# Kernel optimization log

Hardware: AMD Instinct MI355X
Metric: run time of the kernel (lower is better)

The kernel has to match this reference:

```python
import jax, jax.numpy as jnp
import numpy as np

N = 100000   # nodes
E = 220000   # directed edges (each branch)
H = 128      # hidden_dim
OUT = 1      # output_dim
G = 4096     # num graphs in batch
PE = 5       # laplacian eigenvector PE dims
VOCAB = 28   # atom types


def gcn_conv(x, src, dst, W, b, n):
    # PyG GCNConv: x' = D^-1/2 (A + I) D^-1/2 (X W) + b
    h = x @ W
    deg = jax.ops.segment_sum(jnp.ones(src.shape[0], x.dtype), dst, num_segments=n) + 1.0
    dinv = jax.lax.rsqrt(deg)
    coef = dinv[src] * dinv[dst]                                    # [E]
    agg = jax.ops.segment_sum(h[src] * coef[:, None], dst, num_segments=n)
    agg = agg + h * (dinv * dinv)[:, None]                          # self-loop term
    return agg + b


def gcn2(x, edge_index, W1, b1, W2, b2, n):
    # PyG GCN model, num_layers=2: conv -> relu -> conv
    src, dst = edge_index[0], edge_index[1]
    h = jax.nn.relu(gcn_conv(x, src, dst, W1, b1, n))
    return gcn_conv(h, src, dst, W2, b2, n)


def setup_inputs() -> dict:
    key = jax.random.key(0)
    ks = jax.random.split(key, 16)
    s = 0.1
    return {
        "node_tokens": jax.random.randint(ks[0], (N, 1), 0, VOCAB),
        "pe": jax.random.normal(ks[1], (N, PE), jnp.float32),
        "edge_index": jax.random.randint(ks[2], (2, E), 0, N),
        "vr_edge_index": jax.random.randint(ks[3], (2, E), 0, N),
        "batch": jnp.sort(jax.random.randint(ks[4], (N,), 0, G)),
        "embed_table": jax.random.normal(ks[5], (VOCAB, H), jnp.float32) * s,
        "Wt": jax.random.normal(ks[6], (PE, H), jnp.float32) * s,
        "bt": jnp.zeros((H,), jnp.float32),
        "W1": jax.random.normal(ks[7], (H, H), jnp.float32) * s,
        "b1": jnp.zeros((H,), jnp.float32),
        "W2": jax.random.normal(ks[8], (H, OUT), jnp.float32) * s,
        "b2": jnp.zeros((OUT,), jnp.float32),
        "Wv1": jax.random.normal(ks[9], (H, H), jnp.float32) * s,
        "bv1": jnp.zeros((H,), jnp.float32),
        "Wv2": jax.random.normal(ks[10], (H, OUT), jnp.float32) * s,
        "bv2": jnp.zeros((OUT,), jnp.float32),
    }


def reference(node_tokens, pe, edge_index, vr_edge_index, batch, embed_table,
              Wt, bt, W1, b1, W2, b2, Wv1, bv1, Wv2, bv2):
    # embed_x(data.x.long()).squeeze(1) + lin_trans(pe)
    x = embed_table[node_tokens[:, 0]] + (pe @ Wt + bt)             # [N, H]
    x1 = gcn2(x, edge_index, W1, b1, W2, b2, N)                     # [N, OUT]
    xv = gcn2(x, vr_edge_index, Wv1, bv1, Wv2, bv2, N)              # [N, OUT]
    x1 = x1 + xv
    y_hat = jax.ops.segment_sum(x1, batch, num_segments=G)          # [G, OUT]
    y_hat = jnp.squeeze(y_hat, axis=-1)                             # [G]
    return (y_hat, x)
```

## Files before the change

### kernel.cpp

```cpp
#include <hip/hip_runtime.h>

#define NN 100000
#define NE 220000
#define HD 128
#define NG 4096
#define NPE 5
#define NB_SCAN ((NN + 255) / 256)
#define NBX4 ((NN * HD / 4) / 256)
#define NT16 (NN / 16)
#define NBGEMM 1024
#define NBW 128
#define NBZ ((2 * NN + 255) / 256)
#define NBE2 14
#define NBD ((2 * NE + 255) / 256)

typedef unsigned int uint;
typedef unsigned short ushort;
typedef __attribute__((ext_vector_type(8))) short bf16x8;
typedef __attribute__((ext_vector_type(4))) float f32x4;

__device__ __forceinline__ float bf2f(uint u16) {
    return __uint_as_float(u16 << 16);
}
__device__ __forceinline__ ushort f2bf(float f) {
    uint u = __float_as_uint(f);
    u += 0x7fffu + ((u >> 16) & 1u);
    return (ushort)(u >> 16);
}

__global__ void k_prep0(const float* __restrict__ W1, const float* __restrict__ Wv1,
                        const float* __restrict__ embed, const float* __restrict__ bt,
                        ushort* __restrict__ Wcat, int* __restrict__ cnt,
                        float* __restrict__ embed2) {
    int b = blockIdx.x;
    if (b < NBW) {
        int t = b * 256 + threadIdx.x;
        int f = t >> 7, k = t & 127;
        const float* W = (f < HD) ? W1 : Wv1;
        Wcat[t] = f2bf(W[k * HD + (f & 127)]);
    } else if (b < NBW + NBZ) {
        int t = (b - NBW) * 256 + threadIdx.x;
        if (t < 2 * NN) cnt[t] = 0;
    } else {
        int t = (b - NBW - NBZ) * 256 + threadIdx.x;
        if (t < 28 * 128) embed2[t] = embed[t] + bt[t & 127];
    }
}

__global__ void k_front(const int* __restrict__ tok, const float* __restrict__ pe,
                        const float* __restrict__ embed2, const float* __restrict__ Wtr,
                        float* __restrict__ x, ushort* __restrict__ xb,
                        const int* __restrict__ ei, const int* __restrict__ vei,
                        int* __restrict__ cnt, int* __restrict__ rank) {
    int b = blockIdx.x;
    if (b < NBX4) {
        int idx = b * 256 + threadIdx.x;
        int n = idx >> 5, q = idx & 31;
        int t = tok[n];
        float4 acc = ((const float4*)(embed2 + (size_t)t * HD))[q];
        const float* pen = pe + n * NPE;
#pragma unroll
        for (int k = 0; k < NPE; ++k) {
            float p = pen[k];
            float4 wv = ((const float4*)(Wtr + k * HD))[q];
            acc.x += p * wv.x; acc.y += p * wv.y;
            acc.z += p * wv.z; acc.w += p * wv.w;
        }
        ((float4*)x)[idx] = acc;
        uint2 pk;
        pk.x = (uint)f2bf(acc.x) | ((uint)f2bf(acc.y) << 16);
        pk.y = (uint)f2bf(acc.z) | ((uint)f2bf(acc.w) << 16);
        ((uint2*)xb)[idx] = pk;
    } else {
        int t = (b - NBX4) * 256 + threadIdx.x;
        if (t < 2 * NE) {
            int br = t >= NE;
            int e = t - br * NE;
            const int* S = br ? vei : ei;
            rank[t] = atomicAdd(&cnt[br * NN + S[NE + e]], 1);
        }
    }
}

__global__ __launch_bounds__(256) void k_gemm_scan1(
        const ushort* __restrict__ xb, const ushort* __restrict__ Wt,
        ushort* __restrict__ H,
        const int* __restrict__ cnt, int* __restrict__ off,
        int* __restrict__ bsum, float* __restrict__ dinv, float* __restrict__ y) {
    __shared__ int s[256];
    int b = blockIdx.x;
    if (b < 2 * NB_SCAN) {
        int tid = threadIdx.x;
        int gid = b * 256 + tid;
        if (gid < NG) y[gid] = 0.f;
        int br = b / NB_SCAN;
        int blk = b % NB_SCAN;
        int i = blk * 256 + tid;
        int v = (i < NN) ? cnt[br * NN + i] : 0;
        if (i < NN) dinv[br * NN + i] = rsqrtf((float)v + 1.0f);
        s[tid] = v;
        __syncthreads();
        for (int d = 1; d < 256; d <<= 1) {
            int t = (tid >= d) ? s[tid - d] : 0;
            __syncthreads();
            s[tid] += t;
            __syncthreads();
        }
        if (i < NN) off[br * NN + i] = s[tid] - v;
        if (tid == 255) bsum[br * 512 + blk] = s[255];
    } else {
        int w = threadIdx.x >> 6;
        int lane = threadIdx.x & 63;
        int m = lane & 15, quad = lane >> 4;
        const ushort* Wbase = Wt + ((size_t)(w * 4) * 16 + m) * 128 + quad * 8;
        bf16x8 wf[4][4];
#pragma unroll
        for (int j = 0; j < 4; ++j)
#pragma unroll
            for (int kc = 0; kc < 4; ++kc)
                wf[j][kc] = *(const bf16x8*)(Wbase + (size_t)j * 16 * 128 + kc * 32);

        for (int t = b - 2 * NB_SCAN; t < NT16; t += NBGEMM) {
            int n = t * 16 + m;
            const ushort* Arow = xb + (size_t)n * HD + quad * 8;
            bf16x8 xf[4];
#pragma unroll
            for (int kc = 0; kc < 4; ++kc)
                xf[kc] = *(const bf16x8*)(Arow + kc * 32);
            f32x4 acc[4] = {};
#pragma unroll
            for (int j = 0; j < 4; ++j)
#pragma unroll
                for (int kc = 0; kc < 4; ++kc)
                    acc[j] = __builtin_amdgcn_mfma_f32_16x16x32_bf16(wf[j][kc], xf[kc],
                                                                     acc[j], 0, 0, 0);
#pragma unroll
            for (int j = 0; j < 4; ++j) {
                f32x4 a = acc[j];
                uint2 pk;
                pk.x = (uint)f2bf(a[0]) | ((uint)f2bf(a[1]) << 16);
                pk.y = (uint)f2bf(a[2]) | ((uint)f2bf(a[3]) << 16);
                *(uint2*)&H[(size_t)n * 256 + (w * 4 + j) * 16 + quad * 4] = pk;
            }
        }
    }
}

__global__ void k_scan3(const int* __restrict__ off, const int* __restrict__ bsum,
                        const int* __restrict__ cnt, int2* __restrict__ off2) {
    __shared__ int s[256];
    int br = blockIdx.x / NB_SCAN;
    int blk = blockIdx.x % NB_SCAN;
    int tid = threadIdx.x;
    int v = 0;
    if (tid < blk) v = bsum[br * 512 + tid];
    if (tid + 256 < blk) v += bsum[br * 512 + tid + 256];
    s[tid] = v;
#pragma unroll
    for (int d = 128; d > 0; d >>= 1) {
        __syncthreads();
        if (tid < d) s[tid] += s[tid + d];
    }
    __syncthreads();
    int pre = s[0];
    int i = blk * 256 + tid;
    if (i < NN) {
        int o = off[br * NN + i] + pre;
        int2 pr;
        pr.x = o;
        pr.y = o + cnt[br * NN + i];
        off2[br * NN + i] = pr;
    }
}

__global__ void k_scatter(const int* __restrict__ ei, const int* __restrict__ vei,
                          const int* __restrict__ rank, const float* __restrict__ dinv,
                          const int2* __restrict__ off2, int2* __restrict__ ent) {
    int t = blockIdx.x * blockDim.x + threadIdx.x;
    if (t >= 2 * NE) return;
    int br = t >= NE;
    int e = t - br * NE;
    const int* S = br ? vei : ei;
    int s = S[e], d = S[NE + e];
    int pos = off2[br * NN + d].x + rank[t];
    int2 rec;
    rec.x = s;
    rec.y = __float_as_int(dinv[br * NN + s] * dinv[br * NN + d]);
    ent[br * NE + pos] = rec;
}

__global__ void k_gather_ep(const ushort* __restrict__ H, const float* __restrict__ dinv,
                            const int2* __restrict__ off2,
                            const int2* __restrict__ ent,
                            const float* __restrict__ b1, const float* __restrict__ bv1,
                            const float* __restrict__ W2, const float* __restrict__ Wv2,
                            float* __restrict__ z) {
    int wid = threadIdx.x >> 6;
    int lane = threadIdx.x & 63;
    int half = lane >> 5;
    int l = lane & 31;
    int task = blockIdx.x * 8 + wid * 2 + half;
    int br = task >= NN;
    int n = task - br * NN;

    const int2* en = ent + br * NE;
    size_t hoff = (size_t)br * 128;

    int2 pr = off2[br * NN + n];
    int p0 = pr.x, p1 = pr.y;

    float dv = dinv[br * NN + n];
    uint2 u = *(const uint2*)(H + (size_t)n * 256 + hoff + l * 4);
    float c = dv * dv;
    float a0 = bf2f(u.x & 0xffffu) * c, a1 = bf2f(u.x >> 16) * c;
    float a2 = bf2f(u.y & 0xffffu) * c, a3 = bf2f(u.y >> 16) * c;

    for (int p = p0; p < p1; p += 4) {
        int2 e0 = en[p], e1 = en[p + 1], e2 = en[p + 2], e3 = en[p + 3];
        int s0 = e0.x;
        int s1 = (p + 1 < p1) ? e1.x : n;
        int s2 = (p + 2 < p1) ? e2.x : n;
        int s3 = (p + 3 < p1) ? e3.x : n;
        float c0 = __int_as_float(e0.y);
        float c1 = (p + 1 < p1) ? __int_as_float(e1.y) : 0.f;
        float c2 = (p + 2 < p1) ? __int_as_float(e2.y) : 0.f;
        float c3 = (p + 3 < p1) ? __int_as_float(e3.y) : 0.f;
        uint2 v0 = *(const uint2*)(H + (size_t)s0 * 256 + hoff + l * 4);
        uint2 v1 = *(const uint2*)(H + (size_t)s1 * 256 + hoff + l * 4);
        uint2 v2 = *(const uint2*)(H + (size_t)s2 * 256 + hoff + l * 4);
        uint2 v3 = *(const uint2*)(H + (size_t)s3 * 256 + hoff + l * 4);
        a0 += bf2f(v0.x & 0xffffu) * c0; a1 += bf2f(v0.x >> 16) * c0;
        a2 += bf2f(v0.y & 0xffffu) * c0; a3 += bf2f(v0.y >> 16) * c0;
        a0 += bf2f(v1.x & 0xffffu) * c1; a1 += bf2f(v1.x >> 16) * c1;
        a2 += bf2f(v1.y & 0xffffu) * c1; a3 += bf2f(v1.y >> 16) * c1;
        a0 += bf2f(v2.x & 0xffffu) * c2; a1 += bf2f(v2.x >> 16) * c2;
        a2 += bf2f(v2.y & 0xffffu) * c2; a3 += bf2f(v2.y >> 16) * c2;
        a0 += bf2f(v3.x & 0xffffu) * c3; a1 += bf2f(v3.x >> 16) * c3;
        a2 += bf2f(v3.y & 0xffffu) * c3; a3 += bf2f(v3.y >> 16) * c3;
    }

    const float* bb = br ? bv1 : b1;
    const float* ww = br ? Wv2 : W2;
    float4 b4 = *(const float4*)&bb[l * 4];
    float4 w4 = *(const float4*)&ww[l * 4];
    float part = fmaxf(a0 + b4.x, 0.f) * w4.x + fmaxf(a1 + b4.y, 0.f) * w4.y
               + fmaxf(a2 + b4.z, 0.f) * w4.z + fmaxf(a3 + b4.w, 0.f) * w4.w;
#pragma unroll
    for (int o = 16; o > 0; o >>= 1) part += __shfl_down(part, o, 32);
    if (l == 0) z[br * NN + n] = part;
}

__global__ void k_final2(const float* __restrict__ z, const float* __restrict__ dinv,
                         const int2* __restrict__ off2,
                         const int2* __restrict__ ent,
                         const float* __restrict__ b2, const float* __restrict__ bv2,
                         const int* __restrict__ batch, float* __restrict__ y) {
    __shared__ float ybuf[256];
    __shared__ int gbase_s;
    int br = blockIdx.x >= NB_SCAN;
    int nb = blockIdx.x - br * NB_SCAN;
    int tid = threadIdx.x;
    ybuf[tid] = 0.f;
    if (tid == 0) gbase_s = batch[nb * 256];
    __syncthreads();
    int gbase = gbase_s;
    int n = nb * 256 + tid;
    if (n < NN) {
        const int2* en = ent + br * NE;
        float dv = dinv[br * NN + n];
        float acc = z[br * NN + n] * dv * dv;
        int2 pr = off2[br * NN + n];
        int p1 = pr.y;
        for (int p = pr.x; p < p1; p += 4) {
            int2 e0 = en[p], e1 = en[p + 1], e2 = en[p + 2], e3 = en[p + 3];
            int s0 = e0.x;
            int s1 = (p + 1 < p1) ? e1.x : n;
            int s2 = (p + 2 < p1) ? e2.x : n;
            int s3 = (p + 3 < p1) ? e3.x : n;
            float c0 = __int_as_float(e0.y);
            float c1 = (p + 1 < p1) ? __int_as_float(e1.y) : 0.f;
            float c2 = (p + 2 < p1) ? __int_as_float(e2.y) : 0.f;
            float c3 = (p + 3 < p1) ? __int_as_float(e3.y) : 0.f;
            acc += c0 * z[br * NN + s0] + c1 * z[br * NN + s1]
                 + c2 * z[br * NN + s2] + c3 * z[br * NN + s3];
        }
        acc += br ? bv2[0] : b2[0];
        int gi = batch[n] - gbase;
        if (gi < 256) atomicAdd(&ybuf[gi], acc);
        else atomicAdd(&y[batch[n]], acc);
    }
    __syncthreads();
    float v = ybuf[tid];
    if (v != 0.f) atomicAdd(&y[gbase + tid], v);
}

extern "C" void kernel_launch(void* const* d_in, const int* in_sizes, int n_in,
                              void* d_out, int out_size, void* d_ws, size_t ws_size,
                              hipStream_t stream) {
    const int*   tok   = (const int*)d_in[0];
    const float* pe    = (const float*)d_in[1];
    const int*   ei    = (const int*)d_in[2];
    const int*   vei   = (const int*)d_in[3];
    const int*   batch = (const int*)d_in[4];
    const float* embed = (const float*)d_in[5];
    const float* Wtr   = (const float*)d_in[6];
    const float* bt    = (const float*)d_in[7];
    const float* W1    = (const float*)d_in[8];
    const float* b1    = (const float*)d_in[9];
    const float* W2    = (const float*)d_in[10];
    const float* b2    = (const float*)d_in[11];
    const float* Wv1   = (const float*)d_in[12];
    const float* bv1   = (const float*)d_in[13];
    const float* Wv2   = (const float*)d_in[14];
    const float* bv2   = (const float*)d_in[15];

    float* y = (float*)d_out;
    float* x = y + NG;

    char* w = (char*)d_ws;
    ushort* xb   = (ushort*)w;               w += (size_t)NN * HD * 2;
    ushort* H    = (ushort*)w;               w += (size_t)NN * 256 * 2;
    ushort* Wcat = (ushort*)w;               w += 256 * 128 * 2;
    float*  emb2 = (float*)w;                w += 28 * 128 * 4;
    float*  dinv = (float*)w;                w += 2 * NN * 4;
    float*  z    = (float*)w;                w += 2 * NN * 4;
    int*    cnt  = (int*)w;                  w += 2 * NN * 4;
    int*    off  = (int*)w;                  w += 2 * NN * 4;
    int*    rank = (int*)w;                  w += (size_t)2 * NE * 4;
    int2*   off2 = (int2*)w;                 w += (size_t)2 * NN * 8;
    int2*   ent  = (int2*)w;                 w += (size_t)(2 * NE + 8) * 8;
    int*    bsum = (int*)w;                  w += 2 * 512 * 4;

    k_prep0<<<NBW + NBZ + NBE2, 256, 0, stream>>>(W1, Wv1, embed, bt, Wcat, cnt, emb2);
    k_front<<<NBX4 + NBD, 256, 0, stream>>>(tok, pe, emb2, Wtr, x, xb, ei, vei,
                                            cnt, rank);
    k_gemm_scan1<<<2 * NB_SCAN + NBGEMM, 256, 0, stream>>>(xb, Wcat, H,
                                                           cnt, off, bsum, dinv, y);
    k_scan3<<<2 * NB_SCAN, 256, 0, stream>>>(off, bsum, cnt, off2);
    k_scatter<<<NBD, 256, 0, stream>>>(ei, vei, rank, dinv, off2, ent);
    k_gather_ep<<<2 * NN / 8, 256, 0, stream>>>(H, dinv, off2, ent,
                                                b1, bv1, W2, Wv2, z);
    k_final2<<<2 * NB_SCAN, 256, 0, stream>>>(z, dinv, off2, ent,
                                              b2, bv2, batch, y);
}
```

Baseline: 223.0 us.

## Remove prep kernel and bf16 staging; convert x and weights inside GEMM

Drops the separate prep kernel. The counter zeroing becomes a hipMemsetAsync, the embedding bias add moves into the front kernel, and the weight transpose to bf16 is done per wave inside the GEMM, reading strided fp32 weights. The front kernel no longer writes a bf16 copy of x and handles two nodes per thread. The GEMM instead reads fp32 x and converts it to bf16 in registers. This removes one launch and the bf16 x round trip, at the cost of doubled x read traffic in the GEMM and uncoalesced weight loads repeated in each GEMM block.

New measurement: 230.0 us. 3.1% more time.

```diff
diff --git a/kernel.cpp b/kernel.cpp
--- a/kernel.cpp
+++ b/kernel.cpp
@@ -6,12 +6,9 @@
 #define NG 4096
 #define NPE 5
 #define NB_SCAN ((NN + 255) / 256)
-#define NBX4 ((NN * HD / 4) / 256)
+#define NBXH ((NN * HD / 8) / 256)
 #define NT16 (NN / 16)
 #define NBGEMM 1024
-#define NBW 128
-#define NBZ ((2 * NN + 255) / 256)
-#define NBE2 14
 #define NBD ((2 * NE + 255) / 256)
 
 typedef unsigned int uint;
@@ -28,51 +25,38 @@
     return (ushort)(u >> 16);
 }
 
-__global__ void k_prep0(const float* __restrict__ W1, const float* __restrict__ Wv1,
+__global__ void k_front(const int* __restrict__ tok, const float* __restrict__ pe,
                         const float* __restrict__ embed, const float* __restrict__ bt,
-                        ushort* __restrict__ Wcat, int* __restrict__ cnt,
-                        float* __restrict__ embed2) {
-    int b = blockIdx.x;
-    if (b < NBW) {
-        int t = b * 256 + threadIdx.x;
-        int f = t >> 7, k = t & 127;
-        const float* W = (f < HD) ? W1 : Wv1;
-        Wcat[t] = f2bf(W[k * HD + (f & 127)]);
-    } else if (b < NBW + NBZ) {
-        int t = (b - NBW) * 256 + threadIdx.x;
-        if (t < 2 * NN) cnt[t] = 0;
-    } else {
-        int t = (b - NBW - NBZ) * 256 + threadIdx.x;
-        if (t < 28 * 128) embed2[t] = embed[t] + bt[t & 127];
-    }
-}
-
-__global__ void k_front(const int* __restrict__ tok, const float* __restrict__ pe,
-                        const float* __restrict__ embed2, const float* __restrict__ Wtr,
-                        float* __restrict__ x, ushort* __restrict__ xb,
+                        const float* __restrict__ Wtr,
+                        float* __restrict__ x,
                         const int* __restrict__ ei, const int* __restrict__ vei,
                         int* __restrict__ cnt, int* __restrict__ rank) {
     int b = blockIdx.x;
-    if (b < NBX4) {
-        int idx = b * 256 + threadIdx.x;
-        int n = idx >> 5, q = idx & 31;
-        int t = tok[n];
-        float4 acc = ((const float4*)(embed2 + (size_t)t * HD))[q];
-        const float* pen = pe + n * NPE;
+    if (b < NBXH) {
+        int idx0 = b * 256 + threadIdx.x;
+        int idx1 = idx0 + NBXH * 256;
+        int n0 = idx0 >> 5, n1 = idx1 >> 5, q = idx0 & 31;
+        int t0 = tok[n0], t1 = tok[n1];
+        float4 a0 = ((const float4*)(embed + (size_t)t0 * HD))[q];
+        float4 a1 = ((const float4*)(embed + (size_t)t1 * HD))[q];
+        float4 bv = ((const float4*)bt)[q];
+        a0.x += bv.x; a0.y += bv.y; a0.z += bv.z; a0.w += bv.w;
+        a1.x += bv.x; a1.y += bv.y; a1.z += bv.z; a1.w += bv.w;
+        const float* p0 = pe + n0 * NPE;
+        const float* p1 = pe + n1 * NPE;
 #pragma unroll
         for (int k = 0; k < NPE; ++k) {
-            float p = pen[k];
+            float s0 = p0[k], s1 = p1[k];
             float4 wv = ((const float4*)(Wtr + k * HD))[q];
-            acc.x += p * wv.x; acc.y += p * wv.y;
-            acc.z += p * wv.z; acc.w += p * wv.w;
-        }
-        ((float4*)x)[idx] = acc;
-        uint2 pk;
-        pk.x = (uint)f2bf(acc.x) | ((uint)f2bf(acc.y) << 16);
-        pk.y = (uint)f2bf(acc.z) | ((uint)f2bf(acc.w) << 16);
-        ((uint2*)xb)[idx] = pk;
+            a0.x += s0 * wv.x; a0.y += s0 * wv.y;
+            a0.z += s0 * wv.z; a0.w += s0 * wv.w;
+            a1.x += s1 * wv.x; a1.y += s1 * wv.y;
+            a1.z += s1 * wv.z; a1.w += s1 * wv.w;
+        }
+        ((float4*)x)[idx0] = a0;
+        ((float4*)x)[idx1] = a1;
     } else {
-        int t = (b - NBX4) * 256 + threadIdx.x;
+        int t = (b - NBXH) * 256 + threadIdx.x;
         if (t < 2 * NE) {
             int br = t >= NE;
             int e = t - br * NE;
@@ -83,7 +67,8 @@
 }
 
 __global__ __launch_bounds__(256) void k_gemm_scan1(
-        const ushort* __restrict__ xb, const ushort* __restrict__ Wt,
+        const float* __restrict__ x,
+        const float* __restrict__ W1, const float* __restrict__ Wv1,
         ushort* __restrict__ H,
         const int* __restrict__ cnt, int* __restrict__ off,
         int* __restrict__ bsum, float* __restrict__ dinv, float* __restrict__ y) {
@@ -112,21 +97,33 @@
         int w = threadIdx.x >> 6;
         int lane = threadIdx.x & 63;
         int m = lane & 15, quad = lane >> 4;
-        const ushort* Wbase = Wt + ((size_t)(w * 4) * 16 + m) * 128 + quad * 8;
+        const float* Wsrc = (w < 2) ? W1 : Wv1;
+        int fl = (w & 1) * 64 + m;
         bf16x8 wf[4][4];
 #pragma unroll
         for (int j = 0; j < 4; ++j)
 #pragma unroll
-            for (int kc = 0; kc < 4; ++kc)
-                wf[j][kc] = *(const bf16x8*)(Wbase + (size_t)j * 16 * 128 + kc * 32);
+            for (int kc = 0; kc < 4; ++kc) {
+                int kb = quad * 8 + kc * 32;
+                int fc = fl + j * 16;
+#pragma unroll
+                for (int i = 0; i < 8; ++i)
+                    wf[j][kc][i] = (short)f2bf(Wsrc[(size_t)(kb + i) * HD + fc]);
+            }
 
         for (int t = b - 2 * NB_SCAN; t < NT16; t += NBGEMM) {
             int n = t * 16 + m;
-            const ushort* Arow = xb + (size_t)n * HD + quad * 8;
+            const float* Arow = x + (size_t)n * HD + quad * 8;
             bf16x8 xf[4];
 #pragma unroll
-            for (int kc = 0; kc < 4; ++kc)
-                xf[kc] = *(const bf16x8*)(Arow + kc * 32);
+            for (int kc = 0; kc < 4; ++kc) {
+                float4 lo = *(const float4*)(Arow + kc * 32);
+                float4 hi = *(const float4*)(Arow + kc * 32 + 4);
+                xf[kc][0] = (short)f2bf(lo.x); xf[kc][1] = (short)f2bf(lo.y);
+                xf[kc][2] = (short)f2bf(lo.z); xf[kc][3] = (short)f2bf(lo.w);
+                xf[kc][4] = (short)f2bf(hi.x); xf[kc][5] = (short)f2bf(hi.y);
+                xf[kc][6] = (short)f2bf(hi.z); xf[kc][7] = (short)f2bf(hi.w);
+            }
             f32x4 acc[4] = {};
 #pragma unroll
             for (int j = 0; j < 4; ++j)
@@ -318,10 +315,7 @@
     float* x = y + NG;
 
     char* w = (char*)d_ws;
-    ushort* xb   = (ushort*)w;               w += (size_t)NN * HD * 2;
     ushort* H    = (ushort*)w;               w += (size_t)NN * 256 * 2;
-    ushort* Wcat = (ushort*)w;               w += 256 * 128 * 2;
-    float*  emb2 = (float*)w;                w += 28 * 128 * 4;
     float*  dinv = (float*)w;                w += 2 * NN * 4;
     float*  z    = (float*)w;                w += 2 * NN * 4;
     int*    cnt  = (int*)w;                  w += 2 * NN * 4;
@@ -331,10 +325,11 @@
     int2*   ent  = (int2*)w;                 w += (size_t)(2 * NE + 8) * 8;
     int*    bsum = (int*)w;                  w += 2 * 512 * 4;
 
-    k_prep0<<<NBW + NBZ + NBE2, 256, 0, stream>>>(W1, Wv1, embed, bt, Wcat, cnt, emb2);
-    k_front<<<NBX4 + NBD, 256, 0, stream>>>(tok, pe, emb2, Wtr, x, xb, ei, vei,
+    hipMemsetAsync(cnt, 0, 2 * NN * sizeof(int), stream);
+
+    k_front<<<NBXH + NBD, 256, 0, stream>>>(tok, pe, embed, bt, Wtr, x, ei, vei,
                                             cnt, rank);
-    k_gemm_scan1<<<2 * NB_SCAN + NBGEMM, 256, 0, stream>>>(xb, Wcat, H,
+    k_gemm_scan1<<<2 * NB_SCAN + NBGEMM, 256, 0, stream>>>(x, W1, Wv1, H,
                                                            cnt, off, bsum, dinv, y);
     k_scan3<<<2 * NB_SCAN, 256, 0, stream>>>(off, bsum, cnt, off2);
     k_scatter<<<NBD, 256, 0, stream>>>(ei, vei, rank, dinv, off2, ent);
```
